# Performance work log

Hardware: AMD Instinct MI355X
Metric: run time of the kernel (lower is better)

The kernel has to match this reference:

```python
import jax, jax.numpy as jnp
import numpy as np

N_NODES = 50000
N_EDGES = 1600000
IN_FEAT, H_FEAT, OUT_FEAT, N_CLASSES = 256, 128, 64, 8


def setup_inputs() -> dict:
    key = jax.random.key(0)
    ks = jax.random.split(key, 8)
    seq = jax.random.normal(ks[0], (N_NODES, IN_FEAT), dtype=jnp.float32)
    edge_index = jax.random.randint(ks[1], (2, N_EDGES), 0, N_NODES, dtype=jnp.int64)
    # GCNConv weights (stored as [in, out]) and biases; Glorot-ish scale
    W1 = jax.random.normal(ks[2], (IN_FEAT, H_FEAT), dtype=jnp.float32) / np.sqrt(IN_FEAT)
    b1 = jnp.zeros((H_FEAT,), dtype=jnp.float32)
    W2 = jax.random.normal(ks[3], (H_FEAT, OUT_FEAT), dtype=jnp.float32) / np.sqrt(H_FEAT)
    b2 = jnp.zeros((OUT_FEAT,), dtype=jnp.float32)
    Wc = jax.random.normal(ks[4], (OUT_FEAT, N_CLASSES), dtype=jnp.float32) / np.sqrt(OUT_FEAT)
    bc = jnp.zeros((N_CLASSES,), dtype=jnp.float32)
    return {"seq": seq, "edge_index": edge_index,
            "W1": W1, "b1": b1, "W2": W2, "b2": b2, "Wc": Wc, "bc": bc}


def _gcn_conv(x, W, b, src, dst, norm, n_nodes):
    # PyG GCNConv: h = x @ W, then symmetric-normalized aggregation to dst, + bias
    h = x @ W                                   # [N, out]
    msg = h[src] * norm[:, None]                # [E+N, out] gather + scale
    out = jax.ops.segment_sum(msg, dst, num_segments=n_nodes)  # scatter-add
    return out + b


def reference(seq, edge_index, W1, b1, W2, b2, Wc, bc):
    n = seq.shape[0]
    loops = jnp.arange(n, dtype=edge_index.dtype)
    src = jnp.concatenate([edge_index[0], loops])  # add self-loops
    dst = jnp.concatenate([edge_index[1], loops])
    # symmetric normalization deg^{-1/2}[src] * deg^{-1/2}[dst]
    deg = jax.ops.segment_sum(jnp.ones_like(dst, dtype=seq.dtype), dst, num_segments=n)
    dinv = jnp.where(deg > 0, jax.lax.rsqrt(deg), 0.0)
    norm = dinv[src] * dinv[dst]                  # [E+N]
    res1 = _gcn_conv(seq, W1, b1, src, dst, norm, n)
    res2 = _gcn_conv(res1, W2, b2, src, dst, norm, n)
    return res2 @ Wc + bc
```

## Files before the change

### kernel.cpp

```cpp
#include <hip/hip_runtime.h>
#include <hip/hip_bf16.h>
#include <stdint.h>

#define NN 50000
#define NE 1600000
#define BSH 7
#define NBK 391
#define CAP 4608
#define NSB 256
#define ECH 6250
#define NYB 1563

__global__ __launch_bounds__(256) void k_iw(const float* __restrict__ W1, const float* __restrict__ b1,
                                            const float* __restrict__ W2, const float* __restrict__ b2,
                                            const float* __restrict__ Wc, const float* __restrict__ bc,
                                            float* __restrict__ Wcombo, float* __restrict__ c12,
                                            const int* __restrict__ dst, int* __restrict__ bh){
  __shared__ float M1[128 * 8];
  __shared__ int h[4 * NBK];
  const int t = threadIdx.x;
  if (blockIdx.x < 9){
    for (int idx = t; idx < 1024; idx += 256){
      int k = idx >> 3, c = idx & 7;
      float s = 0.f;
      for (int j = 0; j < 64; ++j) s += W2[k * 64 + j] * Wc[j * 8 + c];
      M1[idx] = s;
    }
    __syncthreads();
    if (blockIdx.x < 8){
      int i = blockIdx.x * 32 + (t >> 3), c = t & 7;
      float s = 0.f;
      for (int k = 0; k < 128; ++k) s += W1[i * 128 + k] * M1[k * 8 + c];
      Wcombo[i * 8 + c] = s;
    } else {
      if (t < 8){
        float s = 0.f;
        for (int k = 0; k < 128; ++k) s += b1[k] * M1[k * 8 + t];
        c12[t] = s;
      } else if (t < 16){
        int c = t - 8;
        float s = bc[c];
        for (int k = 0; k < 64; ++k) s += b2[k] * Wc[k * 8 + c];
        c12[t] = s;
      }
    }
  } else {
    const int hb = blockIdx.x - 9;
    for (int i = t; i < 4 * NBK; i += 256) h[i] = 0;
    __syncthreads();
    const int wv = (t >> 6) * NBK;
    const int e0 = hb * ECH;
    for (int e = e0 + t; e < e0 + ECH; e += 256)
      atomicAdd(&h[wv + (dst[e] >> BSH)], 1);
    __syncthreads();
    for (int i = t; i < NBK; i += 256)
      bh[(size_t)hb * NBK + i] = h[i] + h[NBK + i] + h[2 * NBK + i] + h[3 * NBK + i];
  }
}

__global__ __launch_bounds__(NSB) void k_bscan(const int* __restrict__ bh, int* __restrict__ boff,
                                               int* __restrict__ btot){
  __shared__ int lds[NSB];
  const int b = blockIdx.x;
  int v = bh[(size_t)threadIdx.x * NBK + b];
  lds[threadIdx.x] = v;
  __syncthreads();
  for (int ofs = 1; ofs < NSB; ofs <<= 1){
    int t = (threadIdx.x >= ofs) ? lds[threadIdx.x - ofs] : 0;
    __syncthreads();
    lds[threadIdx.x] += t;
    __syncthreads();
  }
  boff[(size_t)threadIdx.x * NBK + b] = lds[threadIdx.x] - v;
  if (threadIdx.x == NSB - 1) btot[b] = lds[NSB - 1];
}

__global__ __launch_bounds__(256) void k_sy(const int* __restrict__ src, const int* __restrict__ dst,
                                            const int* __restrict__ boff, uint32_t* __restrict__ ebuf,
                                            const float* __restrict__ X, const float* __restrict__ Wcombo,
                                            float* __restrict__ Yraw){
  __shared__ int ctr[NBK];
  __shared__ float Wl[2048];
  const int t = threadIdx.x;
  if (blockIdx.x < NSB){
    for (int i = t; i < NBK; i += 256)
      ctr[i] = i * CAP + boff[(size_t)blockIdx.x * NBK + i];
    __syncthreads();
    const int e0 = blockIdx.x * ECH;
    for (int e = e0 + t; e < e0 + ECH; e += 256){
      int d = dst[e];
      int s = src[e];
      int p = atomicAdd(&ctr[d >> BSH], 1);
      ebuf[p] = ((uint32_t)s << 16) | (uint32_t)d;
    }
  } else {
    for (int i = t; i < 2048; i += 256) Wl[i] = Wcombo[i];
    __syncthreads();
    int gid = (blockIdx.x - NSB) * 256 + t;
    int row = gid >> 3, c = gid & 7;
    if (row >= NN) return;
    const float* Xr = X + (size_t)row * 256;
    float acc = 0.f;
    #pragma unroll 8
    for (int k = 0; k < 256; k += 4){
      float4 x = *(const float4*)(Xr + k);
      acc += x.x * Wl[k * 8 + c] + x.y * Wl[(k + 1) * 8 + c]
           + x.z * Wl[(k + 2) * 8 + c] + x.w * Wl[(k + 3) * 8 + c];
    }
    Yraw[(size_t)row * 8 + c] = acc;
  }
}

__global__ __launch_bounds__(256) void k_csr(const uint32_t* __restrict__ ebuf, const int* __restrict__ btot,
                                             float* __restrict__ dinv, int2* __restrict__ offs2,
                                             unsigned short* __restrict__ csr){
  __shared__ uint32_t lede[CAP];
  __shared__ unsigned short lcsr[CAP];
  __shared__ int h[128];
  __shared__ int sb[128];
  const int t = threadIdx.x;
  const int b = blockIdx.x;
  const int base = b * CAP;
  const int cnt = btot[b];
  for (int i = t; i < cnt; i += 256) lede[i] = ebuf[base + i];
  if (t < 128) h[t] = 0;
  __syncthreads();
  for (int i = t; i < cnt; i += 256)
    atomicAdd(&h[lede[i] & 127], 1);
  __syncthreads();
  int deg = (t < 128) ? h[t] : 0;
  for (int ofs = 1; ofs < 128; ofs <<= 1){
    int tv = (t >= ofs && t < 128) ? h[t - ofs] : 0;
    __syncthreads();
    if (t < 128) h[t] += tv;
    __syncthreads();
  }
  int excl = (t < 128) ? (h[t] - deg) : 0;
  int node = (b << BSH) + t;
  if (t < 128 && node < NN){
    dinv[node] = rsqrtf((float)(deg + 1));
    offs2[node] = make_int2(base + excl, base + excl + deg);
  }
  __syncthreads();
  if (t < 128) sb[t] = excl;
  __syncthreads();
  for (int i = t; i < cnt; i += 256){
    uint32_t v = lede[i];
    int p = atomicAdd(&sb[v & 127], 1);
    lcsr[p] = (unsigned short)(v >> 16);
  }
  __syncthreads();
  uint32_t* dstw = (uint32_t*)(csr + base);
  const uint32_t* srcw = (const uint32_t*)lcsr;
  int nw = (cnt + 1) >> 1;
  for (int i = t; i < nw; i += 256) dstw[i] = srcw[i];
}

__global__ __launch_bounds__(256) void k_agg1(const unsigned short* __restrict__ csr, const int2* __restrict__ offs2,
                                              const float* __restrict__ dinv, const float* __restrict__ Y,
                                              float* __restrict__ U, float* __restrict__ V){
  int gid = blockIdx.x * 256 + threadIdx.x;
  int node = gid >> 3, c = gid & 7;
  if (node >= NN) return;
  int2 oe = offs2[node];
  int e = oe.x;
  const int e1 = oe.y;
  float a = 0.f, vd = 0.f;
  for (; e + 4 <= e1; e += 4){
    int s0 = csr[e], s1 = csr[e + 1], s2 = csr[e + 2], s3 = csr[e + 3];
    float d0 = dinv[s0], d1 = dinv[s1], d2 = dinv[s2], d3 = dinv[s3];
    float y0 = Y[(size_t)s0 * 8 + c], y1 = Y[(size_t)s1 * 8 + c];
    float y2 = Y[(size_t)s2 * 8 + c], y3 = Y[(size_t)s3 * 8 + c];
    a += (d0 * y0 + d1 * y1) + (d2 * y2 + d3 * y3);
    vd += (d0 + d1) + (d2 + d3);
  }
  for (; e < e1; ++e){
    int s0 = csr[e];
    float d0 = dinv[s0];
    a += d0 * Y[(size_t)s0 * 8 + c];
    vd += d0;
  }
  float di = dinv[node];
  U[(size_t)node * 8 + c] = di * di * (a + di * Y[(size_t)node * 8 + c]);
  if (c == 0) V[node] = di * (vd + di);
}

__global__ __launch_bounds__(256) void k_agg2(const unsigned short* __restrict__ csr, const int2* __restrict__ offs2,
                                              const float* __restrict__ dinv, const float* __restrict__ U,
                                              const float* __restrict__ V, const float* __restrict__ c12,
                                              float* __restrict__ O){
  int gid = blockIdx.x * 256 + threadIdx.x;
  int node = gid >> 3, c = gid & 7;
  if (node >= NN) return;
  int2 oe = offs2[node];
  int e = oe.x;
  const int e1 = oe.y;
  float a = 0.f;
  for (; e + 4 <= e1; e += 4){
    int s0 = csr[e], s1 = csr[e + 1], s2 = csr[e + 2], s3 = csr[e + 3];
    float y0 = U[(size_t)s0 * 8 + c], y1 = U[(size_t)s1 * 8 + c];
    float y2 = U[(size_t)s2 * 8 + c], y3 = U[(size_t)s3 * 8 + c];
    a += (y0 + y1) + (y2 + y3);
  }
  for (; e < e1; ++e){
    int s0 = csr[e];
    a += U[(size_t)s0 * 8 + c];
  }
  float di = dinv[node];
  O[(size_t)node * 8 + c] = di * (a + U[(size_t)node * 8 + c]) + V[node] * c12[c] + c12[8 + c];
}

extern "C" void kernel_launch(void* const* d_in, const int* in_sizes, int n_in,
                              void* d_out, int out_size, void* d_ws, size_t ws_size,
                              hipStream_t stream) {
  const float* seq = (const float*)d_in[0];
  const int*   ei  = (const int*)d_in[1];
  const int*   esrc = ei;
  const int*   edst = ei + NE;
  const float* W1 = (const float*)d_in[2];
  const float* b1 = (const float*)d_in[3];
  const float* W2 = (const float*)d_in[4];
  const float* b2 = (const float*)d_in[5];
  const float* Wc = (const float*)d_in[6];
  const float* bc = (const float*)d_in[7];
  float* out = (float*)d_out;

  char* ws = (char*)d_ws;
  size_t o = 0;
  auto alloc = [&](size_t bytes) -> void* {
    void* p = ws + o;
    o += (bytes + 255) & ~(size_t)255;
    return p;
  };
  int*      bh    = (int*)alloc((size_t)NSB * NBK * 4);
  int*      boff  = (int*)alloc((size_t)NSB * NBK * 4);
  int*      btot  = (int*)alloc((size_t)NBK * 4);
  uint32_t* ebuf  = (uint32_t*)alloc((size_t)NBK * CAP * 4);
  unsigned short* csr = (unsigned short*)alloc((size_t)NBK * CAP * 2);
  int2*     offs2 = (int2*)alloc((size_t)NN * 8);
  float*    dinv  = (float*)alloc((size_t)NN * 4);
  float*    Wcb   = (float*)alloc(2048 * 4);
  float*    c12   = (float*)alloc(16 * 4);
  float*    Yraw  = (float*)alloc((size_t)NN * 8 * 4);
  float*    U     = (float*)alloc((size_t)NN * 8 * 4);
  float*    V     = (float*)alloc((size_t)NN * 4);

  k_iw     <<<9 + NSB, 256, 0, stream>>>(W1, b1, W2, b2, Wc, bc, Wcb, c12, edst, bh);
  k_bscan  <<<NBK, NSB, 0, stream>>>(bh, boff, btot);
  k_sy     <<<NSB + NYB, 256, 0, stream>>>(esrc, edst, boff, ebuf, seq, Wcb, Yraw);
  k_csr    <<<NBK, 256, 0, stream>>>(ebuf, btot, dinv, offs2, csr);
  k_agg1   <<<NYB, 256, 0, stream>>>(csr, offs2, dinv, Yraw, U, V);
  k_agg2   <<<NYB, 256, 0, stream>>>(csr, offs2, dinv, U, V, c12, out);
}
```

Measured before the change: 88.90 us.

## Regroup preprocessing kernels: fuse bucket scan with dense projection, widen blocks

The dense X·Wcombo projection moves out of the scatter kernel and into the bucket-offset scan kernel, which now handles four buckets per 1024-thread block. The edge scatter becomes its own kernel. The histogram and scatter loops read dst/src as int2 pairs, and block sizes grow to 1024 (512 for CSR build). The aim is to balance the fused kernels so the dense matmul overlaps the scan rather than the atomic-heavy scatter, and to cut instruction overhead. Larger blocks may reduce occupancy flexibility and raise LDS atomic contention per block.

Result: slower. 93.81 us (+5.5%).

```diff
diff --git a/kernel.cpp b/kernel.cpp
--- a/kernel.cpp
+++ b/kernel.cpp
@@ -9,94 +9,83 @@
 #define CAP 4608
 #define NSB 256
 #define ECH 6250
-#define NYB 1563
-
-__global__ __launch_bounds__(256) void k_iw(const float* __restrict__ W1, const float* __restrict__ b1,
-                                            const float* __restrict__ W2, const float* __restrict__ b2,
-                                            const float* __restrict__ Wc, const float* __restrict__ bc,
-                                            float* __restrict__ Wcombo, float* __restrict__ c12,
-                                            const int* __restrict__ dst, int* __restrict__ bh){
-  __shared__ float M1[128 * 8];
-  __shared__ int h[4 * NBK];
-  const int t = threadIdx.x;
-  if (blockIdx.x < 9){
-    for (int idx = t; idx < 1024; idx += 256){
-      int k = idx >> 3, c = idx & 7;
+#define EPAIR 3125
+
+__global__ __launch_bounds__(1024) void k_iw(const float* __restrict__ W1, const float* __restrict__ b1,
+                                             const float* __restrict__ W2, const float* __restrict__ b2,
+                                             const float* __restrict__ Wc, const float* __restrict__ bc,
+                                             float* __restrict__ Wcombo, float* __restrict__ c12,
+                                             const int* __restrict__ dst, int* __restrict__ bh){
+  const int t = threadIdx.x;
+  if (blockIdx.x == 0){
+    __shared__ float M1[1024];
+    {
+      int k = t >> 3, c = t & 7;
       float s = 0.f;
       for (int j = 0; j < 64; ++j) s += W2[k * 64 + j] * Wc[j * 8 + c];
-      M1[idx] = s;
-    }
-    __syncthreads();
-    if (blockIdx.x < 8){
-      int i = blockIdx.x * 32 + (t >> 3), c = t & 7;
+      M1[t] = s;
+    }
+    __syncthreads();
+    for (int idx = t; idx < 2048; idx += 1024){
+      int i = idx >> 3, c = idx & 7;
       float s = 0.f;
       for (int k = 0; k < 128; ++k) s += W1[i * 128 + k] * M1[k * 8 + c];
-      Wcombo[i * 8 + c] = s;
-    } else {
-      if (t < 8){
-        float s = 0.f;
-        for (int k = 0; k < 128; ++k) s += b1[k] * M1[k * 8 + t];
-        c12[t] = s;
-      } else if (t < 16){
-        int c = t - 8;
-        float s = bc[c];
-        for (int k = 0; k < 64; ++k) s += b2[k] * Wc[k * 8 + c];
-        c12[t] = s;
-      }
+      Wcombo[idx] = s;
+    }
+    if (t < 8){
+      float s = 0.f;
+      for (int k = 0; k < 128; ++k) s += b1[k] * M1[k * 8 + t];
+      c12[t] = s;
+    } else if (t < 16){
+      int c = t - 8;
+      float s = bc[c];
+      for (int k = 0; k < 64; ++k) s += b2[k] * Wc[k * 8 + c];
+      c12[t] = s;
     }
   } else {
-    const int hb = blockIdx.x - 9;
-    for (int i = t; i < 4 * NBK; i += 256) h[i] = 0;
-    __syncthreads();
-    const int wv = (t >> 6) * NBK;
-    const int e0 = hb * ECH;
-    for (int e = e0 + t; e < e0 + ECH; e += 256)
-      atomicAdd(&h[wv + (dst[e] >> BSH)], 1);
-    __syncthreads();
-    for (int i = t; i < NBK; i += 256)
+    __shared__ int h[4 * NBK];
+    const int hb = blockIdx.x - 1;
+    for (int i = t; i < 4 * NBK; i += 1024) h[i] = 0;
+    __syncthreads();
+    const int g = (t >> 8) * NBK;
+    const int2* dp = (const int2*)(dst + hb * ECH);
+    for (int i = t; i < EPAIR; i += 1024){
+      int2 d = dp[i];
+      atomicAdd(&h[g + (d.x >> BSH)], 1);
+      atomicAdd(&h[g + (d.y >> BSH)], 1);
+    }
+    __syncthreads();
+    for (int i = t; i < NBK; i += 1024)
       bh[(size_t)hb * NBK + i] = h[i] + h[NBK + i] + h[2 * NBK + i] + h[3 * NBK + i];
   }
 }
 
-__global__ __launch_bounds__(NSB) void k_bscan(const int* __restrict__ bh, int* __restrict__ boff,
-                                               int* __restrict__ btot){
-  __shared__ int lds[NSB];
-  const int b = blockIdx.x;
-  int v = bh[(size_t)threadIdx.x * NBK + b];
-  lds[threadIdx.x] = v;
-  __syncthreads();
-  for (int ofs = 1; ofs < NSB; ofs <<= 1){
-    int t = (threadIdx.x >= ofs) ? lds[threadIdx.x - ofs] : 0;
-    __syncthreads();
-    lds[threadIdx.x] += t;
-    __syncthreads();
-  }
-  boff[(size_t)threadIdx.x * NBK + b] = lds[threadIdx.x] - v;
-  if (threadIdx.x == NSB - 1) btot[b] = lds[NSB - 1];
-}
-
-__global__ __launch_bounds__(256) void k_sy(const int* __restrict__ src, const int* __restrict__ dst,
-                                            const int* __restrict__ boff, uint32_t* __restrict__ ebuf,
-                                            const float* __restrict__ X, const float* __restrict__ Wcombo,
-                                            float* __restrict__ Yraw){
-  __shared__ int ctr[NBK];
-  __shared__ float Wl[2048];
-  const int t = threadIdx.x;
-  if (blockIdx.x < NSB){
-    for (int i = t; i < NBK; i += 256)
-      ctr[i] = i * CAP + boff[(size_t)blockIdx.x * NBK + i];
-    __syncthreads();
-    const int e0 = blockIdx.x * ECH;
-    for (int e = e0 + t; e < e0 + ECH; e += 256){
-      int d = dst[e];
-      int s = src[e];
-      int p = atomicAdd(&ctr[d >> BSH], 1);
-      ebuf[p] = ((uint32_t)s << 16) | (uint32_t)d;
-    }
+__global__ __launch_bounds__(1024) void k_by(const int* __restrict__ bh, int* __restrict__ boff,
+                                             int* __restrict__ btot,
+                                             const float* __restrict__ X, const float* __restrict__ Wcombo,
+                                             float* __restrict__ Yraw){
+  const int t = threadIdx.x;
+  if (blockIdx.x < 98){
+    __shared__ int lds[1024];
+    const int tt = t & 255;
+    const int b = blockIdx.x * 4 + (t >> 8);
+    const bool ok = b < NBK;
+    int v = ok ? bh[(size_t)tt * NBK + b] : 0;
+    lds[t] = v;
+    __syncthreads();
+    for (int ofs = 1; ofs < 256; ofs <<= 1){
+      int tmp = (tt >= ofs) ? lds[t - ofs] : 0;
+      __syncthreads();
+      lds[t] += tmp;
+      __syncthreads();
+    }
+    if (ok) boff[(size_t)tt * NBK + b] = lds[t] - v;
+    if (ok && tt == 255) btot[b] = lds[t];
   } else {
-    for (int i = t; i < 2048; i += 256) Wl[i] = Wcombo[i];
-    __syncthreads();
-    int gid = (blockIdx.x - NSB) * 256 + t;
+    __shared__ float Wl[2048];
+    for (int i = t; i < 2048; i += 1024) Wl[i] = Wcombo[i];
+    __syncthreads();
+    int gid = (blockIdx.x - 98) * 1024 + t;
     int row = gid >> 3, c = gid & 7;
     if (row >= NN) return;
     const float* Xr = X + (size_t)row * 256;
@@ -111,7 +100,26 @@
   }
 }
 
-__global__ __launch_bounds__(256) void k_csr(const uint32_t* __restrict__ ebuf, const int* __restrict__ btot,
+__global__ __launch_bounds__(1024) void k_scat(const int* __restrict__ src, const int* __restrict__ dst,
+                                               const int* __restrict__ boff, uint32_t* __restrict__ ebuf){
+  __shared__ int ctr[NBK];
+  const int t = threadIdx.x;
+  for (int i = t; i < NBK; i += 1024)
+    ctr[i] = i * CAP + boff[(size_t)blockIdx.x * NBK + i];
+  __syncthreads();
+  const int2* dp = (const int2*)(dst + blockIdx.x * ECH);
+  const int2* sp = (const int2*)(src + blockIdx.x * ECH);
+  for (int i = t; i < EPAIR; i += 1024){
+    int2 d = dp[i];
+    int2 s = sp[i];
+    int p0 = atomicAdd(&ctr[d.x >> BSH], 1);
+    ebuf[p0] = ((uint32_t)s.x << 16) | (uint32_t)d.x;
+    int p1 = atomicAdd(&ctr[d.y >> BSH], 1);
+    ebuf[p1] = ((uint32_t)s.y << 16) | (uint32_t)d.y;
+  }
+}
+
+__global__ __launch_bounds__(512) void k_csr(const uint32_t* __restrict__ ebuf, const int* __restrict__ btot,
                                              float* __restrict__ dinv, int2* __restrict__ offs2,
                                              unsigned short* __restrict__ csr){
   __shared__ uint32_t lede[CAP];
@@ -122,10 +130,10 @@
   const int b = blockIdx.x;
   const int base = b * CAP;
   const int cnt = btot[b];
-  for (int i = t; i < cnt; i += 256) lede[i] = ebuf[base + i];
+  for (int i = t; i < cnt; i += 512) lede[i] = ebuf[base + i];
   if (t < 128) h[t] = 0;
   __syncthreads();
-  for (int i = t; i < cnt; i += 256)
+  for (int i = t; i < cnt; i += 512)
     atomicAdd(&h[lede[i] & 127], 1);
   __syncthreads();
   int deg = (t < 128) ? h[t] : 0;
@@ -144,7 +152,7 @@
   __syncthreads();
   if (t < 128) sb[t] = excl;
   __syncthreads();
-  for (int i = t; i < cnt; i += 256){
+  for (int i = t; i < cnt; i += 512){
     uint32_t v = lede[i];
     int p = atomicAdd(&sb[v & 127], 1);
     lcsr[p] = (unsigned short)(v >> 16);
@@ -153,7 +161,7 @@
   uint32_t* dstw = (uint32_t*)(csr + base);
   const uint32_t* srcw = (const uint32_t*)lcsr;
   int nw = (cnt + 1) >> 1;
-  for (int i = t; i < nw; i += 256) dstw[i] = srcw[i];
+  for (int i = t; i < nw; i += 512) dstw[i] = srcw[i];
 }
 
 __global__ __launch_bounds__(256) void k_agg1(const unsigned short* __restrict__ csr, const int2* __restrict__ offs2,
@@ -245,10 +253,10 @@
   float*    U     = (float*)alloc((size_t)NN * 8 * 4);
   float*    V     = (float*)alloc((size_t)NN * 4);
 
-  k_iw     <<<9 + NSB, 256, 0, stream>>>(W1, b1, W2, b2, Wc, bc, Wcb, c12, edst, bh);
-  k_bscan  <<<NBK, NSB, 0, stream>>>(bh, boff, btot);
-  k_sy     <<<NSB + NYB, 256, 0, stream>>>(esrc, edst, boff, ebuf, seq, Wcb, Yraw);
-  k_csr    <<<NBK, 256, 0, stream>>>(ebuf, btot, dinv, offs2, csr);
-  k_agg1   <<<NYB, 256, 0, stream>>>(csr, offs2, dinv, Yraw, U, V);
-  k_agg2   <<<NYB, 256, 0, stream>>>(csr, offs2, dinv, U, V, c12, out);
-}
+  k_iw     <<<1 + NSB, 1024, 0, stream>>>(W1, b1, W2, b2, Wc, bc, Wcb, c12, edst, bh);
+  k_by     <<<98 + 391, 1024, 0, stream>>>(bh, boff, btot, seq, Wcb, Yraw);
+  k_scat   <<<NSB, 1024, 0, stream>>>(esrc, edst, boff, ebuf);
+  k_csr    <<<NBK, 512, 0, stream>>>(ebuf, btot, dinv, offs2, csr);
+  k_agg1   <<<1563, 256, 0, stream>>>(csr, offs2, dinv, Yraw, U, V);
+  k_agg2   <<<1563, 256, 0, stream>>>(csr, offs2, dinv, U, V, c12, out);
+}
```
